# Performance work log

Hardware: AMD Instinct MI355X
Metric: run time of the kernel (lower is better)

## Reference

```python
import jax, jax.numpy as jnp
import numpy as np

CUTOFF = 5.0       # module __init__ arg
BOX_L = 40.0       # side of cubic region positions are drawn from (OBC: no box passed)
N_ATOMS = 8192
MAX_PAIRS = 1_048_576  # static bound on directed pairs (expected ~550k)


def setup_inputs() -> dict:
    key = jax.random.key(0)
    positions = jax.random.uniform(key, (N_ATOMS, 3), dtype=jnp.float32) * BOX_L
    return {"positions": positions}


def _pairwise_dist(x):
    # Euclidean distance matrix via the gram trick (avoids [N,N,3] intermediate).
    sq = jnp.sum(x * x, axis=1)
    d2 = sq[:, None] + sq[None, :] - 2.0 * (x @ x.T)
    return jnp.sqrt(jnp.maximum(d2, 0.0))


def _safe_norm(dr):
    # norm with zero-safe gradient (padded pairs have dr == 0)
    d2 = jnp.sum(dr * dr, axis=1)
    ok = d2 > 0
    return jnp.where(ok, jnp.sqrt(jnp.where(ok, d2, 1.0)), 0.0)


def reference(positions):
    n = positions.shape[0]
    dist = _pairwise_dist(positions)                      # [N, N]
    mask = (dist < CUTOFF) & (~jnp.eye(n, dtype=bool))    # exclude self-pairs
    # torch.argwhere equivalent, padded to static size; padding -> (0, 0)
    i, j = jnp.nonzero(mask, size=MAX_PAIRS, fill_value=0)
    pairs = jnp.stack([i, j], axis=1).astype(jnp.int32)   # [MAX_PAIRS, 2]
    # pairs_buffer_scales: 1 where i < j else 0 (padding (0,0) -> 0)
    buffer_scales = (i < j).astype(jnp.int32)
    # pairs_ds (pbc_flag=False): ||r_j - r_i||
    dr = positions[j] - positions[i]                      # [MAX_PAIRS, 3]
    ds = _safe_norm(dr)
    return pairs, buffer_scales, ds
```

## Files before the change

### kernel.cpp

```cpp
#include <hip/hip_runtime.h>

#define MAXP 1048576
#define NATOMS 8192
#define D2_CUT 0x1.8ffffep+4f
#define CINV 0.175f
#define CAP 192

#define W_CELLOFF 0
#define W_SORTID  512
#define W_SORTPOS 16384
#define W_ROWCNT  49152

__device__ __forceinline__ float sq3_nc(float x, float y, float z) {
#pragma clang fp contract(off)
  float a = x * x;
  float b = y * y;
  float c = z * z;
  return (a + b) + c;
}

__device__ __forceinline__ float d2_gram(float xi, float yi, float zi, float sqi,
                                         float xj, float yj, float zj, float sqj) {
#pragma clang fp contract(off)
  float g = xi * xj;
  g = __builtin_fmaf(yi, yj, g);
  g = __builtin_fmaf(zi, zj, g);
  float t = sqi + sqj;
  float d2 = t - 2.0f * g;
  return d2;
}

__device__ __forceinline__ float d2_direct(float xi, float yi, float zi,
                                           float xj, float yj, float zj) {
#pragma clang fp contract(off)
  float dx = xj - xi;
  float dy = yj - yi;
  float dz = zj - zi;
  float a = dx * dx;
  float b = dy * dy;
  float c = dz * dz;
  return (a + b) + c;
}

__device__ __forceinline__ int cellco(float v) {
  int c = (int)(v * CINV);
  return c < 0 ? 0 : (c > 6 ? 6 : c);
}

__global__ __launch_bounds__(1024) void nl_bin(const float* __restrict__ pos,
                                               float* __restrict__ ws) {
  __shared__ int hcnt[343];
  __shared__ int hoff[344];
  __shared__ int hcur[343];
  __shared__ int s[512];
  const int tid = threadIdx.x;
  if (tid < 343) { hcnt[tid] = 0; hcur[tid] = 0; }
  __syncthreads();

  float x[8], y[8], z[8];
  int cl[8];
#pragma unroll
  for (int k = 0; k < 8; ++k) {
    int a = tid + k * 1024;
    x[k] = pos[3 * a]; y[k] = pos[3 * a + 1]; z[k] = pos[3 * a + 2];
    cl[k] = cellco(x[k]) + 7 * cellco(y[k]) + 49 * cellco(z[k]);
    atomicAdd(&hcnt[cl[k]], 1);
  }
  __syncthreads();

  if (tid < 512) s[tid] = (tid < 343) ? hcnt[tid] : 0;
  __syncthreads();
  for (int off = 1; off < 512; off <<= 1) {
    int v = (tid < 512 && tid >= off) ? s[tid - off] : 0;
    __syncthreads();
    if (tid < 512) s[tid] += v;
    __syncthreads();
  }
  if (tid < 343) hoff[tid] = (tid == 0) ? 0 : s[tid - 1];
  if (tid == 343) hoff[343] = NATOMS;
  __syncthreads();
  if (tid < 344) ((int*)(ws + W_CELLOFF))[tid] = hoff[tid];

  int* sortid = (int*)(ws + W_SORTID);
  float4* sortpos = (float4*)(ws + W_SORTPOS);
#pragma unroll
  for (int k = 0; k < 8; ++k) {
    int slot = hoff[cl[k]] + atomicAdd(&hcur[cl[k]], 1);
    sortid[slot] = tid + k * 1024;
    sortpos[slot] = make_float4(x[k], y[k], z[k], sq3_nc(x[k], y[k], z[k]));
  }
}

__global__ __launch_bounds__(256) void nl_count_fill(const float* __restrict__ pos,
                                                     float* __restrict__ out,
                                                     float* __restrict__ ws) {
  float4* o4 = (float4*)out;
  const int b = blockIdx.x;
  o4[b * 512 + threadIdx.x] = make_float4(0.f, 0.f, 0.f, 0.f);
  o4[b * 512 + 256 + threadIdx.x] = make_float4(0.f, 0.f, 0.f, 0.f);

  const int* celloff = (const int*)(ws + W_CELLOFF);
  const int* sortid = (const int*)(ws + W_SORTID);
  const float4* sortpos = (const float4*)(ws + W_SORTPOS);
  int* rowcnt = (int*)(ws + W_ROWCNT);
  const int lane = threadIdx.x & 63;
  const int wave = threadIdx.x >> 6;
  const int row = b * 4 + wave;
  float xi = pos[3 * row], yi = pos[3 * row + 1], zi = pos[3 * row + 2];
  float sqi = sq3_nc(xi, yi, zi);
  int cx = cellco(xi), cy = cellco(yi), cz = cellco(zi);
  int x0 = max(cx - 1, 0), x1 = min(cx + 1, 6);
  int y0 = max(cy - 1, 0), y1 = min(cy + 1, 6);
  int z0 = max(cz - 1, 0), z1 = min(cz + 1, 6);
  int cnt = 0;
  for (int icz = z0; icz <= z1; ++icz)
    for (int icy = y0; icy <= y1; ++icy) {
      int cb = 7 * icy + 49 * icz;
      int s = celloff[cb + x0];
      int e = celloff[cb + x1 + 1];
      for (int bb = s; bb < e; bb += 64) {
        int t = bb + lane;
        bool v = t < e;
        float4 p = v ? sortpos[t] : make_float4(1e30f, 1e30f, 1e30f, 0.f);
        int j = v ? sortid[t] : -1;
        float d2 = d2_gram(xi, yi, zi, sqi, p.x, p.y, p.z, p.w);
        cnt += (v && (d2 < D2_CUT) && (j != row)) ? 1 : 0;
      }
    }
  for (int off = 32; off > 0; off >>= 1) cnt += __shfl_down(cnt, off, 64);
  if (lane == 0) rowcnt[row] = cnt;
}

__global__ __launch_bounds__(256) void nl_write(const float* __restrict__ pos,
                                                float* __restrict__ out,
                                                const float* __restrict__ ws) {
  const int* celloff = (const int*)(ws + W_CELLOFF);
  const int* sortid = (const int*)(ws + W_SORTID);
  const float4* sortpos = (const float4*)(ws + W_SORTPOS);
  const int* rowcnt = (const int*)(ws + W_ROWCNT);
  __shared__ int pfx[NATOMS];
  __shared__ int tsum[256];
  __shared__ int jb[4][CAP];
  __shared__ float db[4][CAP];
  const int tid = threadIdx.x;
  const int lane = tid & 63;
  const int wave = tid >> 6;
  const int row = blockIdx.x * 4 + wave;

  int run = 0;
  for (int k = 0; k < 32; ++k) {
    pfx[tid * 32 + k] = run;
    run += rowcnt[tid * 32 + k];
  }
  tsum[tid] = run;
  __syncthreads();
  for (int off = 1; off < 256; off <<= 1) {
    int v = (tid >= off) ? tsum[tid - off] : 0;
    __syncthreads();
    tsum[tid] += v;
    __syncthreads();
  }

  float xi = pos[3 * row], yi = pos[3 * row + 1], zi = pos[3 * row + 2];
  float sqi = sq3_nc(xi, yi, zi);
  int cx = cellco(xi), cy = cellco(yi), cz = cellco(zi);
  int x0 = max(cx - 1, 0), x1 = min(cx + 1, 6);
  int y0 = max(cy - 1, 0), y1 = min(cy + 1, 6);
  int z0 = max(cz - 1, 0), z1 = min(cz + 1, 6);
  int cnt = 0;
  for (int icz = z0; icz <= z1; ++icz)
    for (int icy = y0; icy <= y1; ++icy) {
      int cb = 7 * icy + 49 * icz;
      int s = celloff[cb + x0];
      int e = celloff[cb + x1 + 1];
      for (int bb = s; bb < e; bb += 64) {
        int t = bb + lane;
        bool v = t < e;
        float4 p = v ? sortpos[t] : make_float4(1e30f, 1e30f, 1e30f, 0.f);
        int j = v ? sortid[t] : -1;
        float d2 = d2_gram(xi, yi, zi, sqi, p.x, p.y, p.z, p.w);
        bool pred = v && (d2 < D2_CUT) && (j != row);
        unsigned long long m = __ballot(pred ? 1 : 0);
        if (pred) {
          int ps = cnt + __popcll(m & ((1ull << lane) - 1ull));
          if (ps < CAP) {
            jb[wave][ps] = j;
            db[wave][ps] = sqrtf(d2_direct(xi, yi, zi, p.x, p.y, p.z));
          }
        }
        cnt += __popcll(m);
      }
    }
  __syncthreads();

  int k = cnt > CAP ? CAP : cnt;
  int base = pfx[row] + ((row >= 32) ? tsum[(row >> 5) - 1] : 0);
  for (int midx = lane; midx < k; midx += 64) {
    int jm = jb[wave][midx];
    int rank = 0;
    for (int t = 0; t < k; ++t) rank += (jb[wave][t] < jm) ? 1 : 0;
    int idx = base + rank;
    if (idx < MAXP) {
      ((float2*)out)[idx] = make_float2((float)row, (float)jm);
      out[2 * MAXP + idx] = (row < jm) ? 1.0f : 0.0f;
      out[3 * MAXP + idx] = db[wave][midx];
    }
  }
}

extern "C" void kernel_launch(void* const* d_in, const int* in_sizes, int n_in,
                              void* d_out, int out_size, void* d_ws, size_t ws_size,
                              hipStream_t stream) {
  const float* pos = (const float*)d_in[0];
  float* out = (float*)d_out;
  float* ws = (float*)d_ws;

  nl_bin<<<1, 1024, 0, stream>>>(pos, ws);
  nl_count_fill<<<2048, 256, 0, stream>>>(pos, out, ws);
  nl_write<<<2048, 256, 0, stream>>>(pos, out, ws);
}
```

Before: 109.8 us.

## Replace global cell sort with per-cell blocks gathering neighbor candidates into LDS

Drops the single-block binning kernel. Each of 343 blocks now owns one cell: it scans all atoms, collects those in the 27 neighboring cells into shared memory, and evaluates the rows of its own cell against that local candidate list. The row prefix sum moves into a dedicated one-block scan kernel, so write blocks no longer each rebuild a full 8192-entry prefix. The trade-off is that every block rereads all positions, grid parallelism drops to 343 blocks, and new capacity caps (CANDCAP, ROWCAP) would drop pairs if a cell grows unusually dense.

Measured after the change: 159.1 us. 45.0% more time.

```diff
diff --git a/kernel.cpp b/kernel.cpp
--- a/kernel.cpp
+++ b/kernel.cpp
@@ -4,12 +4,13 @@
 #define NATOMS 8192
 #define D2_CUT 0x1.8ffffep+4f
 #define CINV 0.175f
-#define CAP 192
-
-#define W_CELLOFF 0
-#define W_SORTID  512
-#define W_SORTPOS 16384
-#define W_ROWCNT  49152
+#define NCELL 343
+#define CANDCAP 2048
+#define ROWCAP 128
+#define HITCAP 192
+
+#define W_ROWCNT 0
+#define W_ROWOFF 8192
 
 __device__ __forceinline__ float sq3_nc(float x, float y, float z) {
 #pragma clang fp contract(off)
@@ -47,163 +48,161 @@
   return c < 0 ? 0 : (c > 6 ? 6 : c);
 }
 
-__global__ __launch_bounds__(1024) void nl_bin(const float* __restrict__ pos,
-                                               float* __restrict__ ws) {
-  __shared__ int hcnt[343];
-  __shared__ int hoff[344];
-  __shared__ int hcur[343];
-  __shared__ int s[512];
+__global__ __launch_bounds__(256) void nl_count(const float* __restrict__ pos,
+                                                float* __restrict__ out,
+                                                float* __restrict__ ws) {
+  __shared__ float4 cand[CANDCAP];
+  __shared__ int cj[CANDCAP];
+  __shared__ int rows[ROWCAP];
+  __shared__ int ncand, nrows;
   const int tid = threadIdx.x;
-  if (tid < 343) { hcnt[tid] = 0; hcur[tid] = 0; }
-  __syncthreads();
-
-  float x[8], y[8], z[8];
-  int cl[8];
+  const int lane = tid & 63;
+  const int wave = tid >> 6;
+  const int c = blockIdx.x;
+  const int cx = c % 7, cy = (c / 7) % 7, cz = c / 49;
+
+  float4* o4 = (float4*)out;
+  for (int t = c * 256 + tid; t < MAXP; t += NCELL * 256)
+    o4[t] = make_float4(0.f, 0.f, 0.f, 0.f);
+
+  if (tid == 0) { ncand = 0; nrows = 0; }
+  __syncthreads();
+
+  for (int a = tid; a < NATOMS; a += 256) {
+    float x = pos[3 * a], y = pos[3 * a + 1], z = pos[3 * a + 2];
+    int ax = cellco(x), ay = cellco(y), az = cellco(z);
+    int dx = ax - cx, dy = ay - cy, dz = az - cz;
+    if (dx >= -1 && dx <= 1 && dy >= -1 && dy <= 1 && dz >= -1 && dz <= 1) {
+      int p = atomicAdd(&ncand, 1);
+      if (p < CANDCAP) {
+        cand[p] = make_float4(x, y, z, sq3_nc(x, y, z));
+        cj[p] = a;
+      }
+      if (dx == 0 && dy == 0 && dz == 0) {
+        int q = atomicAdd(&nrows, 1);
+        if (q < ROWCAP) rows[q] = a;
+      }
+    }
+  }
+  __syncthreads();
+
+  int* rowcnt = (int*)(ws + W_ROWCNT);
+  const int nc = ncand < CANDCAP ? ncand : CANDCAP;
+  const int nr = nrows < ROWCAP ? nrows : ROWCAP;
+  for (int ri = wave; ri < nr; ri += 4) {
+    int row = rows[ri];
+    float xi = pos[3 * row], yi = pos[3 * row + 1], zi = pos[3 * row + 2];
+    float sqi = sq3_nc(xi, yi, zi);
+    int cnt = 0;
+    for (int b0 = 0; b0 < nc; b0 += 64) {
+      int b = b0 + lane;
+      bool v = b < nc;
+      float4 p = v ? cand[b] : make_float4(1e30f, 1e30f, 1e30f, 0.f);
+      int j = v ? cj[b] : -1;
+      float d2 = d2_gram(xi, yi, zi, sqi, p.x, p.y, p.z, p.w);
+      cnt += (v && (d2 < D2_CUT) && (j != row)) ? 1 : 0;
+    }
+    for (int off = 32; off > 0; off >>= 1) cnt += __shfl_down(cnt, off, 64);
+    if (lane == 0) rowcnt[row] = cnt;
+  }
+}
+
+__global__ __launch_bounds__(1024) void nl_scan(float* __restrict__ ws) {
+  const int* cnts = (const int*)(ws + W_ROWCNT);
+  int* offs = (int*)(ws + W_ROWOFF);
+  __shared__ int s[1024];
+  const int tid = threadIdx.x;
+  const int base = tid * 8;
+  int local[8];
+  int sum = 0;
 #pragma unroll
-  for (int k = 0; k < 8; ++k) {
-    int a = tid + k * 1024;
-    x[k] = pos[3 * a]; y[k] = pos[3 * a + 1]; z[k] = pos[3 * a + 2];
-    cl[k] = cellco(x[k]) + 7 * cellco(y[k]) + 49 * cellco(z[k]);
-    atomicAdd(&hcnt[cl[k]], 1);
-  }
-  __syncthreads();
-
-  if (tid < 512) s[tid] = (tid < 343) ? hcnt[tid] : 0;
-  __syncthreads();
-  for (int off = 1; off < 512; off <<= 1) {
-    int v = (tid < 512 && tid >= off) ? s[tid - off] : 0;
+  for (int k = 0; k < 8; ++k) { local[k] = sum; sum += cnts[base + k]; }
+  s[tid] = sum;
+  __syncthreads();
+  for (int off = 1; off < 1024; off <<= 1) {
+    int v = (tid >= off) ? s[tid - off] : 0;
     __syncthreads();
-    if (tid < 512) s[tid] += v;
+    s[tid] += v;
     __syncthreads();
   }
-  if (tid < 343) hoff[tid] = (tid == 0) ? 0 : s[tid - 1];
-  if (tid == 343) hoff[343] = NATOMS;
-  __syncthreads();
-  if (tid < 344) ((int*)(ws + W_CELLOFF))[tid] = hoff[tid];
-
-  int* sortid = (int*)(ws + W_SORTID);
-  float4* sortpos = (float4*)(ws + W_SORTPOS);
+  int excl = (tid == 0) ? 0 : s[tid - 1];
 #pragma unroll
-  for (int k = 0; k < 8; ++k) {
-    int slot = hoff[cl[k]] + atomicAdd(&hcur[cl[k]], 1);
-    sortid[slot] = tid + k * 1024;
-    sortpos[slot] = make_float4(x[k], y[k], z[k], sq3_nc(x[k], y[k], z[k]));
-  }
-}
-
-__global__ __launch_bounds__(256) void nl_count_fill(const float* __restrict__ pos,
-                                                     float* __restrict__ out,
-                                                     float* __restrict__ ws) {
-  float4* o4 = (float4*)out;
-  const int b = blockIdx.x;
-  o4[b * 512 + threadIdx.x] = make_float4(0.f, 0.f, 0.f, 0.f);
-  o4[b * 512 + 256 + threadIdx.x] = make_float4(0.f, 0.f, 0.f, 0.f);
-
-  const int* celloff = (const int*)(ws + W_CELLOFF);
-  const int* sortid = (const int*)(ws + W_SORTID);
-  const float4* sortpos = (const float4*)(ws + W_SORTPOS);
-  int* rowcnt = (int*)(ws + W_ROWCNT);
-  const int lane = threadIdx.x & 63;
-  const int wave = threadIdx.x >> 6;
-  const int row = b * 4 + wave;
-  float xi = pos[3 * row], yi = pos[3 * row + 1], zi = pos[3 * row + 2];
-  float sqi = sq3_nc(xi, yi, zi);
-  int cx = cellco(xi), cy = cellco(yi), cz = cellco(zi);
-  int x0 = max(cx - 1, 0), x1 = min(cx + 1, 6);
-  int y0 = max(cy - 1, 0), y1 = min(cy + 1, 6);
-  int z0 = max(cz - 1, 0), z1 = min(cz + 1, 6);
-  int cnt = 0;
-  for (int icz = z0; icz <= z1; ++icz)
-    for (int icy = y0; icy <= y1; ++icy) {
-      int cb = 7 * icy + 49 * icz;
-      int s = celloff[cb + x0];
-      int e = celloff[cb + x1 + 1];
-      for (int bb = s; bb < e; bb += 64) {
-        int t = bb + lane;
-        bool v = t < e;
-        float4 p = v ? sortpos[t] : make_float4(1e30f, 1e30f, 1e30f, 0.f);
-        int j = v ? sortid[t] : -1;
-        float d2 = d2_gram(xi, yi, zi, sqi, p.x, p.y, p.z, p.w);
-        cnt += (v && (d2 < D2_CUT) && (j != row)) ? 1 : 0;
-      }
-    }
-  for (int off = 32; off > 0; off >>= 1) cnt += __shfl_down(cnt, off, 64);
-  if (lane == 0) rowcnt[row] = cnt;
+  for (int k = 0; k < 8; ++k) offs[base + k] = excl + local[k];
 }
 
 __global__ __launch_bounds__(256) void nl_write(const float* __restrict__ pos,
                                                 float* __restrict__ out,
                                                 const float* __restrict__ ws) {
-  const int* celloff = (const int*)(ws + W_CELLOFF);
-  const int* sortid = (const int*)(ws + W_SORTID);
-  const float4* sortpos = (const float4*)(ws + W_SORTPOS);
-  const int* rowcnt = (const int*)(ws + W_ROWCNT);
-  __shared__ int pfx[NATOMS];
-  __shared__ int tsum[256];
-  __shared__ int jb[4][CAP];
-  __shared__ float db[4][CAP];
+  __shared__ float4 cand[CANDCAP];
+  __shared__ int cj[CANDCAP];
+  __shared__ int rows[ROWCAP];
+  __shared__ int jb[4][HITCAP];
+  __shared__ float db[4][HITCAP];
+  __shared__ int ncand, nrows;
   const int tid = threadIdx.x;
   const int lane = tid & 63;
   const int wave = tid >> 6;
-  const int row = blockIdx.x * 4 + wave;
-
-  int run = 0;
-  for (int k = 0; k < 32; ++k) {
-    pfx[tid * 32 + k] = run;
-    run += rowcnt[tid * 32 + k];
-  }
-  tsum[tid] = run;
-  __syncthreads();
-  for (int off = 1; off < 256; off <<= 1) {
-    int v = (tid >= off) ? tsum[tid - off] : 0;
-    __syncthreads();
-    tsum[tid] += v;
-    __syncthreads();
-  }
-
-  float xi = pos[3 * row], yi = pos[3 * row + 1], zi = pos[3 * row + 2];
-  float sqi = sq3_nc(xi, yi, zi);
-  int cx = cellco(xi), cy = cellco(yi), cz = cellco(zi);
-  int x0 = max(cx - 1, 0), x1 = min(cx + 1, 6);
-  int y0 = max(cy - 1, 0), y1 = min(cy + 1, 6);
-  int z0 = max(cz - 1, 0), z1 = min(cz + 1, 6);
-  int cnt = 0;
-  for (int icz = z0; icz <= z1; ++icz)
-    for (int icy = y0; icy <= y1; ++icy) {
-      int cb = 7 * icy + 49 * icz;
-      int s = celloff[cb + x0];
-      int e = celloff[cb + x1 + 1];
-      for (int bb = s; bb < e; bb += 64) {
-        int t = bb + lane;
-        bool v = t < e;
-        float4 p = v ? sortpos[t] : make_float4(1e30f, 1e30f, 1e30f, 0.f);
-        int j = v ? sortid[t] : -1;
-        float d2 = d2_gram(xi, yi, zi, sqi, p.x, p.y, p.z, p.w);
-        bool pred = v && (d2 < D2_CUT) && (j != row);
-        unsigned long long m = __ballot(pred ? 1 : 0);
-        if (pred) {
-          int ps = cnt + __popcll(m & ((1ull << lane) - 1ull));
-          if (ps < CAP) {
-            jb[wave][ps] = j;
-            db[wave][ps] = sqrtf(d2_direct(xi, yi, zi, p.x, p.y, p.z));
-          }
+  const int c = blockIdx.x;
+  const int cx = c % 7, cy = (c / 7) % 7, cz = c / 49;
+
+  if (tid == 0) { ncand = 0; nrows = 0; }
+  __syncthreads();
+
+  for (int a = tid; a < NATOMS; a += 256) {
+    float x = pos[3 * a], y = pos[3 * a + 1], z = pos[3 * a + 2];
+    int ax = cellco(x), ay = cellco(y), az = cellco(z);
+    int dx = ax - cx, dy = ay - cy, dz = az - cz;
+    if (dx >= -1 && dx <= 1 && dy >= -1 && dy <= 1 && dz >= -1 && dz <= 1) {
+      int p = atomicAdd(&ncand, 1);
+      if (p < CANDCAP) {
+        cand[p] = make_float4(x, y, z, sq3_nc(x, y, z));
+        cj[p] = a;
+      }
+      if (dx == 0 && dy == 0 && dz == 0) {
+        int q = atomicAdd(&nrows, 1);
+        if (q < ROWCAP) rows[q] = a;
+      }
+    }
+  }
+  __syncthreads();
+
+  const int* rowoff = (const int*)(ws + W_ROWOFF);
+  const int nc = ncand < CANDCAP ? ncand : CANDCAP;
+  const int nr = nrows < ROWCAP ? nrows : ROWCAP;
+  for (int ri = wave; ri < nr; ri += 4) {
+    int row = rows[ri];
+    float xi = pos[3 * row], yi = pos[3 * row + 1], zi = pos[3 * row + 2];
+    float sqi = sq3_nc(xi, yi, zi);
+    int cnt = 0;
+    for (int b0 = 0; b0 < nc; b0 += 64) {
+      int b = b0 + lane;
+      bool v = b < nc;
+      float4 p = v ? cand[b] : make_float4(1e30f, 1e30f, 1e30f, 0.f);
+      int j = v ? cj[b] : -1;
+      float d2 = d2_gram(xi, yi, zi, sqi, p.x, p.y, p.z, p.w);
+      bool pred = v && (d2 < D2_CUT) && (j != row);
+      unsigned long long m = __ballot(pred ? 1 : 0);
+      if (pred) {
+        int ps = cnt + __popcll(m & ((1ull << lane) - 1ull));
+        if (ps < HITCAP) {
+          jb[wave][ps] = j;
+          db[wave][ps] = sqrtf(d2_direct(xi, yi, zi, p.x, p.y, p.z));
         }
-        cnt += __popcll(m);
-      }
-    }
-  __syncthreads();
-
-  int k = cnt > CAP ? CAP : cnt;
-  int base = pfx[row] + ((row >= 32) ? tsum[(row >> 5) - 1] : 0);
-  for (int midx = lane; midx < k; midx += 64) {
-    int jm = jb[wave][midx];
-    int rank = 0;
-    for (int t = 0; t < k; ++t) rank += (jb[wave][t] < jm) ? 1 : 0;
-    int idx = base + rank;
-    if (idx < MAXP) {
-      ((float2*)out)[idx] = make_float2((float)row, (float)jm);
-      out[2 * MAXP + idx] = (row < jm) ? 1.0f : 0.0f;
-      out[3 * MAXP + idx] = db[wave][midx];
+      }
+      cnt += __popcll(m);
+    }
+    int k = cnt > HITCAP ? HITCAP : cnt;
+    int base = rowoff[row];
+    for (int midx = lane; midx < k; midx += 64) {
+      int jm = jb[wave][midx];
+      int rank = 0;
+      for (int t = 0; t < k; ++t) rank += (jb[wave][t] < jm) ? 1 : 0;
+      int idx = base + rank;
+      if (idx < MAXP) {
+        ((float2*)out)[idx] = make_float2((float)row, (float)jm);
+        out[2 * MAXP + idx] = (row < jm) ? 1.0f : 0.0f;
+        out[3 * MAXP + idx] = db[wave][midx];
+      }
     }
   }
 }
@@ -215,7 +214,7 @@
   float* out = (float*)d_out;
   float* ws = (float*)d_ws;
 
-  nl_bin<<<1, 1024, 0, stream>>>(pos, ws);
-  nl_count_fill<<<2048, 256, 0, stream>>>(pos, out, ws);
-  nl_write<<<2048, 256, 0, stream>>>(pos, out, ws);
-}
+  nl_count<<<NCELL, 256, 0, stream>>>(pos, out, ws);
+  nl_scan<<<1, 1024, 0, stream>>>(ws);
+  nl_write<<<NCELL, 256, 0, stream>>>(pos, out, ws);
+}
```

## Move per-block redundant row prefix scan into a dedicated single-block scan kernel

Applied to the files above, without the earlier changes.

Previously every one of 2048 write blocks reloaded all 8192 row counts and ran a full prefix scan in shared memory (32 KB pfx array plus multiple barriers). A separate single-block scan kernel now computes row offsets once into the workspace, and the write kernel just reads its offset. This drops redundant global reads, shared memory use and barriers per block, which should raise occupancy, at the cost of an extra kernel launch. The workspace layout is also rearranged.

Result: faster. 100.7 us (-8.2%).

```diff
diff --git a/kernel.cpp b/kernel.cpp
--- a/kernel.cpp
+++ b/kernel.cpp
@@ -8,8 +8,9 @@
 
 #define W_CELLOFF 0
 #define W_SORTID  512
-#define W_SORTPOS 16384
-#define W_ROWCNT  49152
+#define W_ROWCNT  8704
+#define W_ROWOFF  16896
+#define W_SORTPOS 25088
 
 __device__ __forceinline__ float sq3_nc(float x, float y, float z) {
 #pragma clang fp contract(off)
@@ -47,8 +48,8 @@
   return c < 0 ? 0 : (c > 6 ? 6 : c);
 }
 
-__global__ __launch_bounds__(1024) void nl_bin(const float* __restrict__ pos,
-                                               float* __restrict__ ws) {
+__global__ __launch_bounds__(1024) void nl_prep(const float* __restrict__ pos,
+                                                float* __restrict__ ws) {
   __shared__ int hcnt[343];
   __shared__ int hoff[344];
   __shared__ int hcur[343];
@@ -91,9 +92,9 @@
   }
 }
 
-__global__ __launch_bounds__(256) void nl_count_fill(const float* __restrict__ pos,
-                                                     float* __restrict__ out,
-                                                     float* __restrict__ ws) {
+__global__ __launch_bounds__(256) void nl_rowcount(const float* __restrict__ pos,
+                                                   float* __restrict__ out,
+                                                   float* __restrict__ ws) {
   float4* o4 = (float4*)out;
   const int b = blockIdx.x;
   o4[b * 512 + threadIdx.x] = make_float4(0.f, 0.f, 0.f, 0.f);
@@ -116,11 +117,11 @@
   for (int icz = z0; icz <= z1; ++icz)
     for (int icy = y0; icy <= y1; ++icy) {
       int cb = 7 * icy + 49 * icz;
-      int s = celloff[cb + x0];
-      int e = celloff[cb + x1 + 1];
-      for (int bb = s; bb < e; bb += 64) {
+      int st = celloff[cb + x0];
+      int en = celloff[cb + x1 + 1];
+      for (int bb = st; bb < en; bb += 64) {
         int t = bb + lane;
-        bool v = t < e;
+        bool v = t < en;
         float4 p = v ? sortpos[t] : make_float4(1e30f, 1e30f, 1e30f, 0.f);
         int j = v ? sortid[t] : -1;
         float d2 = d2_gram(xi, yi, zi, sqi, p.x, p.y, p.z, p.w);
@@ -131,36 +132,41 @@
   if (lane == 0) rowcnt[row] = cnt;
 }
 
-__global__ __launch_bounds__(256) void nl_write(const float* __restrict__ pos,
-                                                float* __restrict__ out,
-                                                const float* __restrict__ ws) {
+__global__ __launch_bounds__(1024) void nl_rowscan(float* __restrict__ ws) {
+  const int* cnts = (const int*)(ws + W_ROWCNT);
+  int* offs = (int*)(ws + W_ROWOFF);
+  __shared__ int s[1024];
+  const int tid = threadIdx.x;
+  const int base = tid * 8;
+  int local[8];
+  int sum = 0;
+#pragma unroll
+  for (int k = 0; k < 8; ++k) { local[k] = sum; sum += cnts[base + k]; }
+  s[tid] = sum;
+  __syncthreads();
+  for (int off = 1; off < 1024; off <<= 1) {
+    int v = (tid >= off) ? s[tid - off] : 0;
+    __syncthreads();
+    s[tid] += v;
+    __syncthreads();
+  }
+  int excl = (tid == 0) ? 0 : s[tid - 1];
+#pragma unroll
+  for (int k = 0; k < 8; ++k) offs[base + k] = excl + local[k];
+}
+
+__global__ __launch_bounds__(256) void nl_rowwrite(const float* __restrict__ pos,
+                                                   float* __restrict__ out,
+                                                   const float* __restrict__ ws) {
   const int* celloff = (const int*)(ws + W_CELLOFF);
   const int* sortid = (const int*)(ws + W_SORTID);
   const float4* sortpos = (const float4*)(ws + W_SORTPOS);
-  const int* rowcnt = (const int*)(ws + W_ROWCNT);
-  __shared__ int pfx[NATOMS];
-  __shared__ int tsum[256];
+  const int* rowoff = (const int*)(ws + W_ROWOFF);
   __shared__ int jb[4][CAP];
   __shared__ float db[4][CAP];
-  const int tid = threadIdx.x;
-  const int lane = tid & 63;
-  const int wave = tid >> 6;
+  const int lane = threadIdx.x & 63;
+  const int wave = threadIdx.x >> 6;
   const int row = blockIdx.x * 4 + wave;
-
-  int run = 0;
-  for (int k = 0; k < 32; ++k) {
-    pfx[tid * 32 + k] = run;
-    run += rowcnt[tid * 32 + k];
-  }
-  tsum[tid] = run;
-  __syncthreads();
-  for (int off = 1; off < 256; off <<= 1) {
-    int v = (tid >= off) ? tsum[tid - off] : 0;
-    __syncthreads();
-    tsum[tid] += v;
-    __syncthreads();
-  }
-
   float xi = pos[3 * row], yi = pos[3 * row + 1], zi = pos[3 * row + 2];
   float sqi = sq3_nc(xi, yi, zi);
   int cx = cellco(xi), cy = cellco(yi), cz = cellco(zi);
@@ -171,11 +177,11 @@
   for (int icz = z0; icz <= z1; ++icz)
     for (int icy = y0; icy <= y1; ++icy) {
       int cb = 7 * icy + 49 * icz;
-      int s = celloff[cb + x0];
-      int e = celloff[cb + x1 + 1];
-      for (int bb = s; bb < e; bb += 64) {
+      int st = celloff[cb + x0];
+      int en = celloff[cb + x1 + 1];
+      for (int bb = st; bb < en; bb += 64) {
         int t = bb + lane;
-        bool v = t < e;
+        bool v = t < en;
         float4 p = v ? sortpos[t] : make_float4(1e30f, 1e30f, 1e30f, 0.f);
         int j = v ? sortid[t] : -1;
         float d2 = d2_gram(xi, yi, zi, sqi, p.x, p.y, p.z, p.w);
@@ -191,10 +197,8 @@
         cnt += __popcll(m);
       }
     }
-  __syncthreads();
-
   int k = cnt > CAP ? CAP : cnt;
-  int base = pfx[row] + ((row >= 32) ? tsum[(row >> 5) - 1] : 0);
+  int base = rowoff[row];
   for (int midx = lane; midx < k; midx += 64) {
     int jm = jb[wave][midx];
     int rank = 0;
@@ -215,7 +219,8 @@
   float* out = (float*)d_out;
   float* ws = (float*)d_ws;
 
-  nl_bin<<<1, 1024, 0, stream>>>(pos, ws);
-  nl_count_fill<<<2048, 256, 0, stream>>>(pos, out, ws);
-  nl_write<<<2048, 256, 0, stream>>>(pos, out, ws);
-}
+  nl_prep<<<1, 1024, 0, stream>>>(pos, ws);
+  nl_rowcount<<<NATOMS / 4, 256, 0, stream>>>(pos, out, ws);
+  nl_rowscan<<<1, 1024, 0, stream>>>(ws);
+  nl_rowwrite<<<NATOMS / 4, 256, 0, stream>>>(pos, out, ws);
+}
```
